# Optimization experiments

Measured on AMD Instinct MI355X. Metric: run time of the kernel, lower is better.

## Reference

```python
import jax, jax.numpy as jnp
import numpy as np

N, D, NUM_CLASSES = 1024, 256, 10
EPS = 1e-12


def setup_inputs() -> dict:
    key = jax.random.key(0)
    k1, k2, k3, k4 = jax.random.split(key, 4)
    return {
        "fm_s": jax.random.normal(k1, (N, D), dtype=jnp.float32),
        "fm_t": jax.random.normal(k2, (N, D), dtype=jnp.float32),
        "logvar_s": jax.random.normal(k3, (N, D), dtype=jnp.float32),
        "targets": jax.random.randint(k4, (N,), 0, NUM_CLASSES, dtype=jnp.int64),
        "fusion_true": 0,  # False branch (no multi_index)
    }


def reference(fm_s, fm_t, logvar_s, targets, fusion_true):
    # pairwise squared diff scaled by per-row (student) variance: (N, N, D)
    diff2 = (fm_s[:, None, :] - fm_t[None, :, :]) ** 2
    inv_var_term = diff2 / (2.0 * jnp.exp(logvar_s)[:, None, :] + EPS)
    half_lv = 0.5 * logvar_s[:, None, :]
    lp = jax.nn.relu(inv_var_term + half_lv).sum(-1)   # (N, N)
    ln = jax.nn.relu(-inv_var_term - half_lv).sum(-1)  # (N, N)
    pos = (targets[:, None] == targets[None, :]).astype(fm_s.dtype)  # self_mask_pos
    neg = 1.0 - pos
    loss_pos = lp * pos / pos.sum(-1, keepdims=True)
    loss_neg = ln * neg / neg.sum(-1, keepdims=True)
    # fusion_true == False path
    return loss_pos.sum(-1).mean() + loss_neg.sum(-1).mean()
```

## Files before the change

### kernel.cpp

```cpp
#include <hip/hip_runtime.h>
#include <math.h>

#define NN   1024
#define DD   256
#define NCLS 10
#define FEPS 1e-12f

#define TI 64
#define TJ 128
#define DC 32
#define DSPLIT 8
#define NBLK ((NN / TI) * (NN / TJ) * DSPLIT)

__device__ __forceinline__ int swq8(int r, int q) {
    return (q + r + (r >> 3)) & 7;
}

__global__ __launch_bounds__(256) void count_kernel(const long long* __restrict__ tgt,
                                                    int* __restrict__ counts) {
    __shared__ int c[NCLS];
    int tid = threadIdx.x;
    if (tid < NCLS) c[tid] = 0;
    __syncthreads();
    for (int k = tid; k < NN; k += 256) atomicAdd(&c[(int)tgt[k]], 1);
    __syncthreads();
    if (tid < NCLS) counts[tid] = c[tid];
}

__global__ __launch_bounds__(256) void pair_kernel(
    const float* __restrict__ fm_s, const float* __restrict__ fm_t,
    const float* __restrict__ lv, const long long* __restrict__ tgt,
    const int* __restrict__ counts, float* __restrict__ partials)
{
    __shared__ float Al[TI * DC];
    __shared__ float Bl[TI * DC];
    __shared__ float Vl[TI * DC];
    __shared__ float Fl[TJ * DC];

    const int bid  = blockIdx.x;
    const int tile = bid >> 3;
    const int kd   = bid & 7;
    const int i0   = (tile >> 3) * TI;
    const int j0   = (tile & 7) * TJ;
    const int doff = kd * DC;

    const int tid  = threadIdx.x;
    const int tx   = tid & 15;
    const int ty   = tid >> 4;
    const int lane = tid & 63;
    const int w    = tid >> 6;
    const int dl   = lane & 31;
    const int rsub = lane >> 5;
    const int ql   = dl >> 2;
    const int el   = dl & 3;

    float s1[4][8], s2[4][8];
#pragma unroll
    for (int a = 0; a < 4; ++a)
#pragma unroll
        for (int b = 0; b < 8; ++b) { s1[a][b] = 0.f; s2[a][b] = 0.f; }

#pragma unroll
    for (int rp = 0; rp < TJ / 8; ++rp) {
        const int r = rp * 8 + w * 2 + rsub;
        Fl[r * DC + swq8(r, ql) * 4 + el] = fm_t[(j0 + r) * DD + doff + dl];
    }
#pragma unroll
    for (int rp = 0; rp < TI / 8; ++rp) {
        const int r = rp * 8 + w * 2 + rsub;
        const int g = (i0 + r) * DD + doff + dl;
        const float fs = fm_s[g];
        const float l  = lv[g];
        const float iv = 1.0f / (2.0f * expf(l) + FEPS);
        const int  a   = r * DC + swq8(r, ql) * 4 + el;
        const float fsiv = fs * iv;
        Al[a] = fmaf(fsiv, fs, 0.5f * l);
        Bl[a] = -2.0f * fsiv;
        Vl[a] = iv;
    }
    __syncthreads();

#pragma unroll 1
    for (int dq = 0; dq < DC / 4; ++dq) {
        float4 fa[4], fb[4], fv[4];
#pragma unroll
        for (int r = 0; r < 4; ++r) {
            const int i = ty * 4 + r;
            const int o = i * DC + swq8(i, dq) * 4;
            fa[r] = *(const float4*)&Al[o];
            fb[r] = *(const float4*)&Bl[o];
            fv[r] = *(const float4*)&Vl[o];
        }
#pragma unroll
        for (int rj = 0; rj < 8; ++rj) {
            const int j = tx * 8 + rj;
            const float4 f = *(const float4*)&Fl[j * DC + swq8(j, dq) * 4];
            const float4 f2 = make_float4(f.x * f.x, f.y * f.y, f.z * f.z, f.w * f.w);
#pragma unroll
            for (int ri = 0; ri < 4; ++ri) {
                const float t0 = fmaf(f2.x, fv[ri].x, fmaf(fb[ri].x, f.x, fa[ri].x));
                const float t1 = fmaf(f2.y, fv[ri].y, fmaf(fb[ri].y, f.y, fa[ri].y));
                const float t2 = fmaf(f2.z, fv[ri].z, fmaf(fb[ri].z, f.z, fa[ri].z));
                const float t3 = fmaf(f2.w, fv[ri].w, fmaf(fb[ri].w, f.w, fa[ri].w));
                s1[ri][rj] += (t0 + t1) + (t2 + t3);
                s2[ri][rj] += (fabsf(t0) + fabsf(t1)) + (fabsf(t2) + fabsf(t3));
            }
        }
    }

    float csum = 0.f;
#pragma unroll
    for (int ri = 0; ri < 4; ++ri) {
        const int ti  = (int)tgt[i0 + ty * 4 + ri];
        const int cnt = counts[ti];
        const float wp = 1.0f / (float)cnt;
        const float wn = 1.0f / (float)(NN - cnt);
#pragma unroll
        for (int rj = 0; rj < 8; ++rj) {
            const int tj = (int)tgt[j0 + tx * 8 + rj];
            const float lp = 0.5f * (s2[ri][rj] + s1[ri][rj]);
            const float ln = 0.5f * (s2[ri][rj] - s1[ri][rj]);
            csum += (ti == tj) ? lp * wp : ln * wn;
        }
    }

#pragma unroll
    for (int off = 32; off > 0; off >>= 1) csum += __shfl_down(csum, off);
    __syncthreads();
    if (lane == 0) Al[w] = csum;
    __syncthreads();
    if (tid == 0) partials[bid] = (Al[0] + Al[1]) + (Al[2] + Al[3]);
}

__global__ __launch_bounds__(256) void finalize_kernel(const float* __restrict__ partials,
                                                       float* __restrict__ out) {
    __shared__ float red[256];
    const int tid = threadIdx.x;
    red[tid] = (partials[tid] + partials[tid + 256]) +
               (partials[tid + 512] + partials[tid + 768]);
    __syncthreads();
    for (int s = 128; s > 0; s >>= 1) {
        if (tid < s) red[tid] += red[tid + s];
        __syncthreads();
    }
    if (tid == 0) out[0] = red[0] * (1.0f / (float)NN);
}

extern "C" void kernel_launch(void* const* d_in, const int* in_sizes, int n_in,
                              void* d_out, int out_size, void* d_ws, size_t ws_size,
                              hipStream_t stream) {
    const float* fm_s    = (const float*)d_in[0];
    const float* fm_t    = (const float*)d_in[1];
    const float* lv      = (const float*)d_in[2];
    const long long* tgt = (const long long*)d_in[3];

    int*   counts   = (int*)d_ws;
    float* partials = (float*)((char*)d_ws + 64);

    hipLaunchKernelGGL(count_kernel, dim3(1), dim3(256), 0, stream, tgt, counts);
    hipLaunchKernelGGL(pair_kernel, dim3(NBLK), dim3(256), 0, stream,
                       fm_s, fm_t, lv, tgt, counts, partials);
    hipLaunchKernelGGL(finalize_kernel, dim3(1), dim3(256), 0, stream,
                       partials, (float*)d_out);
}
```

Measured before the change: 45.81 us.

## Vectorize tile staging, simplify swizzle, use packed FMA and hoist target loads

Staging of fm_t, fm_s and logvar into shared memory now uses float4 global loads and float4 LDS stores with a new XOR-free rotation swizzle, and the inner loop is fully unrolled with precomputed LDS pointers. The inner FMAs are expressed on 2-wide vectors so the compiler can emit packed FP32 FMA instructions. 1/(2exp(l)+eps) is replaced by 0.5*__expf(-l), which drops the eps term and uses the fast exp. Target and count loads are hoisted before the barrier, reading only the low 32 bits of the int64 targets. These target fewer load instructions, less ALU work and better overlap of global loads with the barrier, at the cost of small numerical differences and an assumption of little-endian, non-negative int64 targets.

```diff
diff --git a/kernel.cpp b/kernel.cpp
--- a/kernel.cpp
+++ b/kernel.cpp
@@ -4,7 +4,6 @@
 #define NN   1024
 #define DD   256
 #define NCLS 10
-#define FEPS 1e-12f
 
 #define TI 64
 #define TJ 128
@@ -12,9 +11,8 @@
 #define DSPLIT 8
 #define NBLK ((NN / TI) * (NN / TJ) * DSPLIT)
 
-__device__ __forceinline__ int swq8(int r, int q) {
-    return (q + r + (r >> 3)) & 7;
-}
+typedef float f32x2 __attribute__((ext_vector_type(2)));
+typedef float f32x4 __attribute__((ext_vector_type(4)));
 
 __global__ __launch_bounds__(256) void count_kernel(const long long* __restrict__ tgt,
                                                     int* __restrict__ counts) {
@@ -49,10 +47,51 @@
     const int ty   = tid >> 4;
     const int lane = tid & 63;
     const int w    = tid >> 6;
-    const int dl   = lane & 31;
-    const int rsub = lane >> 5;
-    const int ql   = dl >> 2;
-    const int el   = dl & 3;
+
+    const int srow = tid >> 3;
+    const int sq   = tid & 7;
+#pragma unroll
+    for (int p = 0; p < 4; ++p) {
+        const int r = p * 32 + srow;
+        f32x4 v = *(const f32x4*)&fm_t[(j0 + r) * DD + doff + sq * 4];
+        const int phys = (sq + (r >> 3)) & 7;
+        *(f32x4*)&Fl[r * DC + phys * 4] = v;
+    }
+#pragma unroll
+    for (int p = 0; p < 2; ++p) {
+        const int r = p * 32 + srow;
+        const int g = (i0 + r) * DD + doff + sq * 4;
+        f32x4 fs = *(const f32x4*)&fm_s[g];
+        f32x4 l  = *(const f32x4*)&lv[g];
+        f32x4 A, B, V;
+#pragma unroll
+        for (int e = 0; e < 4; ++e) {
+            const float iv = 0.5f * __expf(-l[e]);
+            const float fsiv = fs[e] * iv;
+            A[e] = fmaf(fsiv, fs[e], 0.5f * l[e]);
+            B[e] = -2.0f * fsiv;
+            V[e] = iv;
+        }
+        const int phys = (sq + (r >> 2)) & 7;
+        *(f32x4*)&Al[r * DC + phys * 4] = A;
+        *(f32x4*)&Bl[r * DC + phys * 4] = B;
+        *(f32x4*)&Vl[r * DC + phys * 4] = V;
+    }
+
+    const int* tgt32 = (const int*)tgt;
+    int ti_r[4], tj_r[8];
+    float wp_r[4], wn_r[4];
+#pragma unroll
+    for (int ri = 0; ri < 4; ++ri) {
+        ti_r[ri] = tgt32[(i0 + ty * 4 + ri) * 2];
+        const int cnt = counts[ti_r[ri]];
+        wp_r[ri] = 1.0f / (float)cnt;
+        wn_r[ri] = 1.0f / (float)(NN - cnt);
+    }
+#pragma unroll
+    for (int rj = 0; rj < 8; ++rj) tj_r[rj] = tgt32[(j0 + tx * 8 + rj) * 2];
+
+    __syncthreads();
 
     float s1[4][8], s2[4][8];
 #pragma unroll
@@ -61,49 +100,32 @@
         for (int b = 0; b < 8; ++b) { s1[a][b] = 0.f; s2[a][b] = 0.f; }
 
 #pragma unroll
-    for (int rp = 0; rp < TJ / 8; ++rp) {
-        const int r = rp * 8 + w * 2 + rsub;
-        Fl[r * DC + swq8(r, ql) * 4 + el] = fm_t[(j0 + r) * DD + doff + dl];
-    }
-#pragma unroll
-    for (int rp = 0; rp < TI / 8; ++rp) {
-        const int r = rp * 8 + w * 2 + rsub;
-        const int g = (i0 + r) * DD + doff + dl;
-        const float fs = fm_s[g];
-        const float l  = lv[g];
-        const float iv = 1.0f / (2.0f * expf(l) + FEPS);
-        const int  a   = r * DC + swq8(r, ql) * 4 + el;
-        const float fsiv = fs * iv;
-        Al[a] = fmaf(fsiv, fs, 0.5f * l);
-        Bl[a] = -2.0f * fsiv;
-        Vl[a] = iv;
-    }
-    __syncthreads();
-
-#pragma unroll 1
-    for (int dq = 0; dq < DC / 4; ++dq) {
-        float4 fa[4], fb[4], fv[4];
+    for (int k = 0; k < 8; ++k) {
+        const int iq = ((k + ty) & 7) * 4;
+        const f32x4* pa = (const f32x4*)&Al[ty * 128 + iq];
+        const f32x4* pb = (const f32x4*)&Bl[ty * 128 + iq];
+        const f32x4* pv = (const f32x4*)&Vl[ty * 128 + iq];
+        f32x4 fa[4], fb[4], fv[4];
 #pragma unroll
         for (int r = 0; r < 4; ++r) {
-            const int i = ty * 4 + r;
-            const int o = i * DC + swq8(i, dq) * 4;
-            fa[r] = *(const float4*)&Al[o];
-            fb[r] = *(const float4*)&Bl[o];
-            fv[r] = *(const float4*)&Vl[o];
+            fa[r] = pa[r * 8];
+            fb[r] = pb[r * 8];
+            fv[r] = pv[r * 8];
         }
+        const f32x4* pf = (const f32x4*)&Fl[tx * 256 + ((k + tx) & 7) * 4];
 #pragma unroll
         for (int rj = 0; rj < 8; ++rj) {
-            const int j = tx * 8 + rj;
-            const float4 f = *(const float4*)&Fl[j * DC + swq8(j, dq) * 4];
-            const float4 f2 = make_float4(f.x * f.x, f.y * f.y, f.z * f.z, f.w * f.w);
+            const f32x4 f = pf[rj * 8];
+            const f32x2 f01 = f.lo, f23 = f.hi;
+            const f32x2 g01 = f01 * f01, g23 = f23 * f23;
 #pragma unroll
             for (int ri = 0; ri < 4; ++ri) {
-                const float t0 = fmaf(f2.x, fv[ri].x, fmaf(fb[ri].x, f.x, fa[ri].x));
-                const float t1 = fmaf(f2.y, fv[ri].y, fmaf(fb[ri].y, f.y, fa[ri].y));
-                const float t2 = fmaf(f2.z, fv[ri].z, fmaf(fb[ri].z, f.z, fa[ri].z));
-                const float t3 = fmaf(f2.w, fv[ri].w, fmaf(fb[ri].w, f.w, fa[ri].w));
-                s1[ri][rj] += (t0 + t1) + (t2 + t3);
-                s2[ri][rj] += (fabsf(t0) + fabsf(t1)) + (fabsf(t2) + fabsf(t3));
+                const f32x2 t01 = __builtin_elementwise_fma(g01, fv[ri].lo,
+                                    __builtin_elementwise_fma(f01, fb[ri].lo, fa[ri].lo));
+                const f32x2 t23 = __builtin_elementwise_fma(g23, fv[ri].hi,
+                                    __builtin_elementwise_fma(f23, fb[ri].hi, fa[ri].hi));
+                s1[ri][rj] += (t01.x + t01.y) + (t23.x + t23.y);
+                s2[ri][rj] += (fabsf(t01.x) + fabsf(t01.y)) + (fabsf(t23.x) + fabsf(t23.y));
             }
         }
     }
@@ -111,16 +133,11 @@
     float csum = 0.f;
 #pragma unroll
     for (int ri = 0; ri < 4; ++ri) {
-        const int ti  = (int)tgt[i0 + ty * 4 + ri];
-        const int cnt = counts[ti];
-        const float wp = 1.0f / (float)cnt;
-        const float wn = 1.0f / (float)(NN - cnt);
 #pragma unroll
         for (int rj = 0; rj < 8; ++rj) {
-            const int tj = (int)tgt[j0 + tx * 8 + rj];
             const float lp = 0.5f * (s2[ri][rj] + s1[ri][rj]);
             const float ln = 0.5f * (s2[ri][rj] - s1[ri][rj]);
-            csum += (ti == tj) ? lp * wp : ln * wn;
+            csum += (ti_r[ri] == tj_r[rj]) ? lp * wp_r[ri] : ln * wn_r[ri];
         }
     }
 
```

Result: faster. 39.02 us (-14.8%).
